# Performance work log

Measured on AMD Instinct MI355X. Metric: run time of the kernel, lower is better.

Reference implementation:

```python
import jax, jax.numpy as jnp
import numpy as np

K = 9        # kNN neighbors (ViG default kernel_size=9)
EPS = 1e-5   # BatchNorm eps


def _bn2d(x, gamma, beta):
    # training-mode BatchNorm2d over (B,H,W) per channel; x: [B,C,H,W]
    mean = jnp.mean(x, axis=(0, 2, 3), keepdims=True)
    var = jnp.var(x, axis=(0, 2, 3), keepdims=True)
    g = gamma.reshape(1, -1, 1, 1)
    b = beta.reshape(1, -1, 1, 1)
    return g * (x - mean) * jax.lax.rsqrt(var + EPS) + b


def setup_inputs() -> dict:
    key = jax.random.key(0)
    B, C, H, W = 8, 96, 56, 56
    oup = 192
    ks = jax.random.split(key, 8)
    sc = 0.05
    return {
        "x": jax.random.normal(ks[0], (B, C, H, W), dtype=jnp.float32),
        "W_fc1": jax.random.normal(ks[1], (C, C), dtype=jnp.float32) * sc,
        "b_fc1": jnp.zeros((C,), jnp.float32),
        "g_bn1": jnp.ones((C,), jnp.float32),
        "be_bn1": jnp.zeros((C,), jnp.float32),
        "W_edge": jax.random.normal(ks[2], (2 * C, 2 * C), dtype=jnp.float32) * sc,
        "b_edge": jnp.zeros((2 * C,), jnp.float32),
        "g_bne": jnp.ones((2 * C,), jnp.float32),
        "be_bne": jnp.zeros((2 * C,), jnp.float32),
        "W_fc2": jax.random.normal(ks[3], (2 * C, C), dtype=jnp.float32) * sc,
        "b_fc2": jnp.zeros((C,), jnp.float32),
        "g_bn2": jnp.ones((C,), jnp.float32),
        "be_bn2": jnp.zeros((C,), jnp.float32),
        "g_sabn": jnp.ones((C,), jnp.float32),
        "be_sabn": jnp.zeros((C,), jnp.float32),
        "W_dw": jax.random.normal(ks[4], (oup, C, 3, 3), dtype=jnp.float32) * sc,
        "b_dw": jnp.zeros((oup,), jnp.float32),
        "g_dwbn": jnp.ones((oup,), jnp.float32),
        "be_dwbn": jnp.zeros((oup,), jnp.float32),
    }


def reference(x, W_fc1, b_fc1, g_bn1, be_bn1, W_edge, b_edge, g_bne, be_bne,
              W_fc2, b_fc2, g_bn2, be_bn2, g_sabn, be_sabn,
              W_dw, b_dw, g_dwbn, be_dwbn):
    B, C, H, W = x.shape
    N = H * W
    shortcut = x

    # --- Grapher.fc1: 1x1 conv + BN ---
    y = jnp.einsum('bchw,cd->bdhw', x, W_fc1) + b_fc1[None, :, None, None]
    y = _bn2d(y, g_bn1, be_bn1)

    # --- dynamic kNN graph over flattened tokens ---
    ft = y.reshape(B, C, N).transpose(0, 2, 1)            # [B,N,C]
    sq = jnp.sum(ft * ft, axis=-1)                        # [B,N]
    dist = sq[:, :, None] - 2.0 * jnp.einsum('bnc,bmc->bnm', ft, ft) + sq[:, None, :]
    _, idx = jax.lax.top_k(-dist, K)                      # [B,N,K] nearest neighbors

    # --- EdgeConv: max_k act(BN(W [x_i, x_j - x_i])) ---
    x_j = jnp.take_along_axis(ft[:, :, None, :], idx[..., None], axis=1)  # [B,N,K,C]
    x_i = ft[:, :, None, :]                               # [B,N,1,C]
    e = jnp.concatenate([jnp.broadcast_to(x_i, x_j.shape), x_j - x_i], axis=-1)  # [B,N,K,2C]
    e = jnp.einsum('bnkc,cd->bnkd', e, W_edge) + b_edge
    m = jnp.mean(e, axis=(0, 1, 2))
    v = jnp.var(e, axis=(0, 1, 2))
    e = g_bne * (e - m) * jax.lax.rsqrt(v + EPS) + be_bne
    e = jax.nn.relu(e)
    g = jnp.max(e, axis=2)                                # [B,N,2C] max-aggregation

    # --- Grapher.fc2: 1x1 conv + BN, residual ---
    g = jnp.einsum('bnc,cd->bnd', g, W_fc2) + b_fc2       # [B,N,C]
    g = g.transpose(0, 2, 1).reshape(B, C, H, W)
    g = _bn2d(g, g_bn2, be_bn2)
    y = g + shortcut

    # --- SAEncoder: BN + ReLU ---
    y = jax.nn.relu(_bn2d(y, g_sabn, be_sabn))

    # --- convdw: 3x3 stride-2 conv + BN + ReLU ---
    y = jax.lax.conv_general_dilated(
        y, W_dw, window_strides=(2, 2), padding=((1, 1), (1, 1)),
        dimension_numbers=('NCHW', 'OIHW', 'NCHW')) + b_dw[None, :, None, None]
    y = jax.nn.relu(_bn2d(y, g_dwbn, be_dwbn))
    return y
```

## Files before the change

kernel.cpp:

```cpp
#include <hip/hip_runtime.h>
#include <math.h>

#define B_   8
#define C_   96
#define C2_  192
#define N_   3136
#define R_   25088
#define OUP_ 192
#define HO_  28
#define NO_  784
#define EPS_ 1e-5f
#define QSTR 104
#define CAP3 64

typedef short bf16x8 __attribute__((ext_vector_type(8)));
typedef float f32x4  __attribute__((ext_vector_type(4)));

__global__ __launch_bounds__(512) void k_fc1_d(const float* __restrict__ x,
                                               const float* __restrict__ W1,
                                               const float* __restrict__ b1,
                                               double* __restrict__ yd) {
    __shared__ double Wl[96 * 48];
    int tid = threadIdx.x;
    int rl = tid & 255, h = tid >> 8;
    int dbase = blockIdx.y * 48;
    for (int q = tid; q < 96 * 48; q += 512) {
        int c = q / 48, dd = q % 48;
        Wl[c * 48 + dd] = (double)W1[c * 96 + dbase + dd];
    }
    __syncthreads();
    int r = blockIdx.x * 256 + rl;
    int b = r / N_;
    int n = r - b * N_;
    double acc[24];
#pragma unroll
    for (int i = 0; i < 24; i++) acc[i] = 0.0;
    const float* xp = x + (size_t)b * C_ * N_ + n;
    for (int c = 0; c < 96; ++c) {
        double xv = (double)xp[(size_t)c * N_];
        const double* w = &Wl[c * 48 + h * 24];
#pragma unroll
        for (int i = 0; i < 24; ++i) acc[i] += xv * w[i];
    }
    int d0 = dbase + h * 24;
#pragma unroll
    for (int i = 0; i < 24; i++) {
        int d = d0 + i;
        yd[((size_t)b * C_ + d) * N_ + n] = acc[i] + (double)b1[d];
    }
}

__global__ __launch_bounds__(256) void k_stats_chan_d(const double* __restrict__ src,
                                                      double* __restrict__ partial) {
    int c = blockIdx.x;
    int chunk = blockIdx.y;
    const int SPLIT = 16;
    double s = 0.0, ss = 0.0;
    for (int j = chunk * 256 + threadIdx.x; j < R_; j += SPLIT * 256) {
        int b = j / N_, n = j - b * N_;
        double v = src[((size_t)b * C_ + c) * N_ + n];
        s += v;
        ss += v * v;
    }
    __shared__ double red[8];
    for (int off = 32; off; off >>= 1) {
        s += __shfl_down(s, off, 64);
        ss += __shfl_down(ss, off, 64);
    }
    int lane = threadIdx.x & 63, w = threadIdx.x >> 6;
    if (lane == 0) { red[w * 2] = s; red[w * 2 + 1] = ss; }
    __syncthreads();
    if (threadIdx.x == 0) {
        s = red[0] + red[2] + red[4] + red[6];
        ss = red[1] + red[3] + red[5] + red[7];
        partial[(c * SPLIT + chunk) * 2] = s;
        partial[(c * SPLIT + chunk) * 2 + 1] = ss;
    }
}

__global__ void k_stats_reduce_d(const double* __restrict__ partial, double* __restrict__ stats) {
    int c = blockIdx.x * blockDim.x + threadIdx.x;
    if (c >= 96) return;
    double s = 0.0, ss = 0.0;
    for (int k = 0; k < 16; k++) {
        s += partial[(c * 16 + k) * 2];
        ss += partial[(c * 16 + k) * 2 + 1];
    }
    double m = s / (double)R_;
    double var = ss / (double)R_ - m * m;
    stats[c * 2] = m;
    stats[c * 2 + 1] = 1.0 / sqrt(var + 1e-5);
}

__global__ __launch_bounds__(256) void k_stats_chan(const float* __restrict__ src,
                                                    float* __restrict__ partial,
                                                    int Cn, int Nsp, int total) {
    int c = blockIdx.x;
    int chunk = blockIdx.y;
    int SPLIT = gridDim.y;
    float s = 0.f, ss = 0.f;
    for (int j = chunk * 256 + threadIdx.x; j < total; j += SPLIT * 256) {
        int b = j / Nsp, n = j - b * Nsp;
        float v = src[((size_t)b * Cn + c) * Nsp + n];
        s += v;
        ss += v * v;
    }
    __shared__ float red[8];
    for (int off = 32; off; off >>= 1) {
        s += __shfl_down(s, off, 64);
        ss += __shfl_down(ss, off, 64);
    }
    int lane = threadIdx.x & 63, w = threadIdx.x >> 6;
    if (lane == 0) { red[w * 2] = s; red[w * 2 + 1] = ss; }
    __syncthreads();
    if (threadIdx.x == 0) {
        s = red[0] + red[2] + red[4] + red[6];
        ss = red[1] + red[3] + red[5] + red[7];
        partial[(c * SPLIT + chunk) * 2] = s;
        partial[(c * SPLIT + chunk) * 2 + 1] = ss;
    }
}

__global__ void k_stats_reduce(const float* __restrict__ partial, float* __restrict__ stats,
                               int Cn, int SPLIT, float invcount) {
    int c = blockIdx.x * blockDim.x + threadIdx.x;
    if (c >= Cn) return;
    float s = 0.f, ss = 0.f;
    for (int k = 0; k < SPLIT; k++) {
        s += partial[(c * SPLIT + k) * 2];
        ss += partial[(c * SPLIT + k) * 2 + 1];
    }
    float m = s * invcount;
    float var = ss * invcount - m * m;
    stats[c * 2] = m;
    stats[c * 2 + 1] = 1.0f / sqrtf(var + EPS_);
}

__global__ __launch_bounds__(256) void k_stats_reduce_b2(const float* __restrict__ partial,
                                                         float* __restrict__ stats,
                                                         float invcount) {
    int c = blockIdx.x;
    float s = 0.f, ss = 0.f;
    for (int k = threadIdx.x; k < 784; k += 256) {
        s  += partial[(size_t)k * 384 + c];
        ss += partial[(size_t)k * 384 + 192 + c];
    }
    __shared__ float red[8];
    for (int off = 32; off; off >>= 1) {
        s += __shfl_down(s, off, 64);
        ss += __shfl_down(ss, off, 64);
    }
    int lane = threadIdx.x & 63, w = threadIdx.x >> 6;
    if (lane == 0) { red[w * 2] = s; red[w * 2 + 1] = ss; }
    __syncthreads();
    if (threadIdx.x == 0) {
        s = red[0] + red[2] + red[4] + red[6];
        ss = red[1] + red[3] + red[5] + red[7];
        float m = s * invcount;
        float var = ss * invcount - m * m;
        stats[c * 2] = m;
        stats[c * 2 + 1] = 1.0f / sqrtf(var + EPS_);
    }
}

__global__ __launch_bounds__(256) void k_bn1_apply_d(const double* __restrict__ yd,
                                                     const double* __restrict__ stats,
                                                     const float* __restrict__ g,
                                                     const float* __restrict__ be,
                                                     float* __restrict__ ftc,
                                                     float* __restrict__ ftp32,
                                                     double* __restrict__ ftp64) {
    int i = blockIdx.x * 256 + threadIdx.x;
    if (i >= B_ * C_ * N_) return;
    int n = i % N_;
    int bc = i / N_;
    int c = bc % C_;
    int b = bc / C_;
    double m = stats[c * 2], rs = stats[c * 2 + 1];
    double v = (double)g[c] * (yd[i] - m) * rs + (double)be[c];
    float vf = (float)v;
    ftc[i] = vf;
    size_t pp = ((size_t)b * N_ + n) * C_ + c;
    ftp32[pp] = vf;
    ftp64[pp] = v;
}

__global__ __launch_bounds__(256) void k_sqrows_d(const double* __restrict__ ftp64,
                                                  double* __restrict__ sq64,
                                                  float* __restrict__ sq32) {
    int r = blockIdx.x * 256 + threadIdx.x;
    if (r >= R_) return;
    const double* p = ftp64 + (size_t)r * C_;
    double s = 0.0;
    for (int q = 0; q < 96; q++) s += p[q] * p[q];
    sq64[r] = s;
    sq32[r] = (float)s;
}

__global__ __launch_bounds__(256) void k_split_h(const float* __restrict__ ftp32,
                                                 unsigned short* __restrict__ fspH) {
    int t = blockIdx.x * 256 + threadIdx.x;
    if (t >= R_ * 12) return;
    int p = t / 12, g = t % 12;
    const float* src = ftp32 + (size_t)p * C_ + g * 8;
    unsigned short hi[8];
#pragma unroll
    for (int j = 0; j < 8; ++j) {
        unsigned u = __float_as_uint(src[j]);
        hi[j] = (unsigned short)((u + 0x7fffu + ((u >> 16) & 1u)) >> 16);
    }
    unsigned short* dh = fspH + (size_t)p * QSTR + g * 8;
    *(ushort4*)dh       = *(ushort4*)&hi[0];
    *(ushort4*)(dh + 4) = *(ushort4*)&hi[4];
}

__global__ __launch_bounds__(256) void k_dist3(const unsigned short* __restrict__ fspH,
                                               const float* __restrict__ sq32,
                                               unsigned short* __restrict__ poolC,
                                               unsigned* __restrict__ poolCnt) {
    __shared__ __align__(16) char lds[42112];
    unsigned short* cminL = (unsigned short*)(lds + 26624);
    unsigned short* poolL = (unsigned short*)(lds + 32896);
    unsigned*       cntL  = (unsigned*)(lds + 41088);
    float*          t16fL = (float*)(lds + 41344);

    int b = blockIdx.y;
    int q0 = blockIdx.x * 64;
    int tid = threadIdx.x;
    int w = tid >> 6, l = tid & 63;
    const int koff = (l >> 4) * 8;

    {
        const uint4* src = (const uint4*)(fspH + ((size_t)b * N_ + q0) * QSTR);
        uint4* dst = (uint4*)(lds + 26624);
        for (int i = tid; i < 832; i += 256) dst[i] = src[i];
    }
    __syncthreads();
    bf16x8 Bq[3];
    {
        const unsigned short* Ql = (const unsigned short*)(lds + 26624);
#pragma unroll
        for (int s = 0; s < 3; ++s)
            Bq[s] = *(const bf16x8*)&Ql[(w * 16 + (l & 15)) * QSTR + s * 32 + koff];
    }
    __syncthreads();

    {
        const uint4* src = (const uint4*)(fspH + ((size_t)b * N_) * QSTR);
        uint4* dst = (uint4*)lds;
#pragma unroll
        for (int k = 0; k < 4; ++k) { int i = tid + k * 256; if (i < 832) dst[i] = src[i]; }
        if (tid < 64) ((float*)(lds + 41600))[tid] = sq32[(size_t)b * N_ + tid];
    }
    __syncthreads();

    float t16r = 0.f;
    int cur = 0;
    for (int t = 0; t < 98; ++t) {
        int ch = (t < 49) ? t : t - 49;
        int c0 = ch * 64;
        bool pf = (t < 97);
        uint4 st0, st1, st2, st3; float sqst = 0.f;
        if (pf) {
            int nch = (t + 1 < 49) ? (t + 1) : (t + 1 - 49);
            const uint4* src = (const uint4*)(fspH + ((size_t)b * N_ + nch * 64) * QSTR);
            st0 = src[tid];
            st1 = src[tid + 256];
            st2 = src[tid + 512];
            if (tid < 64) { st3 = src[tid + 768]; sqst = sq32[(size_t)b * N_ + nch * 64 + tid]; }
        }
        const unsigned short* Bc = (const unsigned short*)(lds + cur * 13312);
        const float* sqc = (const float*)(lds + 41600 + cur * 256);
        f32x4 acc[4];
#pragma unroll
        for (int ct = 0; ct < 4; ++ct) acc[ct] = (f32x4){0.f, 0.f, 0.f, 0.f};
#pragma unroll
        for (int s = 0; s < 3; ++s) {
#pragma unroll
            for (int ct = 0; ct < 4; ++ct) {
                bf16x8 Ac = *(const bf16x8*)&Bc[(ct * 16 + (l & 15)) * QSTR + s * 32 + koff];
                acc[ct] = __builtin_amdgcn_mfma_f32_16x16x32_bf16(Ac, Bq[s], acc[ct], 0, 0, 0);
            }
        }
        f32x4 scn[4];
#pragma unroll
        for (int ct = 0; ct < 4; ++ct) scn[ct] = *(const f32x4*)&sqc[ct * 16 + (l >> 4) * 4];
        if (t < 49) {
            float m = 1e30f;
#pragma unroll
            for (int ct = 0; ct < 4; ++ct)
#pragma unroll
                for (int j = 0; j < 4; ++j)
                    m = fminf(m, fmaf(-2.f, acc[ct][j], scn[ct][j]));
            m = fminf(m, __shfl_xor(m, 16, 64));
            m = fminf(m, __shfl_xor(m, 32, 64));
            if (l < 16) {
                unsigned u = __float_as_uint(m);
                unsigned ku = u ^ (0x80000000u | (unsigned)((int)u >> 31));
                cminL[ch * 64 + w * 16 + l] = (unsigned short)(ku >> 16);
            }
        } else {
            int qrow = w * 16 + (l & 15);
#pragma unroll
            for (int ct = 0; ct < 4; ++ct)
#pragma unroll
                for (int j = 0; j < 4; ++j) {
                    float d = fmaf(-2.f, acc[ct][j], scn[ct][j]);
                    if (d <= t16r) {
                        unsigned pos = atomicAdd(&cntL[qrow], 1u);
                        if (pos < (unsigned)CAP3)
                            poolL[qrow * CAP3 + pos] = (unsigned short)(c0 + ct * 16 + (l >> 4) * 4 + j);
                    }
                }
        }
        if (t == 48) {
            __syncthreads();
            if (tid < 64) {
                unsigned short top[16];
#pragma unroll
                for (int j = 0; j < 16; ++j) top[j] = 0xFFFFu;
                for (int q = 0; q < 49; ++q) {
                    unsigned short v = cminL[q * 64 + tid];
                    if (v < top[15]) {
                        top[15] = v;
#pragma unroll
                        for (int j = 15; j >= 1; --j)
                            if (top[j] < top[j - 1]) { unsigned short tt = top[j]; top[j] = top[j - 1]; top[j - 1] = tt; }
                    }
                }
                unsigned ku = ((unsigned)top[15] << 16) | 0xFFFFu;
                float f = (ku & 0x80000000u) ? __uint_as_float(ku ^ 0x80000000u)
                                             : __uint_as_float(~ku);
                t16fL[tid] = f + fabsf(f) * 0.01f + 1.0f;
                cntL[tid] = 0u;
            }
            __syncthreads();
            t16r = t16fL[w * 16 + (l & 15)];
        }
        if (pf) {
            uint4* dst = (uint4*)(lds + (cur ^ 1) * 13312);
            dst[tid] = st0;
            dst[tid + 256] = st1;
            dst[tid + 512] = st2;
            if (tid < 64) { dst[tid + 768] = st3; ((float*)(lds + 41600 + (cur ^ 1) * 256))[tid] = sqst; }
        }
        __syncthreads();
        cur ^= 1;
    }
    if (tid < 64) {
        unsigned c = cntL[tid];
        poolCnt[(size_t)b * N_ + q0 + tid] = (c > (unsigned)CAP3) ? (unsigned)CAP3 : c;
    }
    {
        unsigned* dst = (unsigned*)(poolC + ((size_t)b * N_ + q0) * CAP3);
        const unsigned* src = (const unsigned*)poolL;
        for (int i = tid; i < 64 * CAP3 / 2; i += 256) dst[i] = src[i];
    }
}

__global__ __launch_bounds__(256) void k_rerank_d(const unsigned short* __restrict__ poolC,
                                                  const unsigned* __restrict__ poolCnt,
                                                  const double* __restrict__ ftp64,
                                                  const double* __restrict__ sq64,
                                                  int* __restrict__ idx) {
    int tid = threadIdx.x;
    int wv = tid >> 6, l = tid & 63;
    int rr = blockIdx.x * 4 + wv;
    int b = rr / N_;
    unsigned cnt = poolCnt[rr];
    if (cnt > (unsigned)CAP3) cnt = CAP3;
    double d = 1e300;
    int j = 0x7fffffff;
    if (l < (int)cnt) {
        j = (int)poolC[(size_t)rr * CAP3 + l];
        const double* qb = ftp64 + (size_t)rr * C_;
        const double* cb = ftp64 + ((size_t)b * N_ + j) * C_;
        double s0 = 0.0, s1 = 0.0;
#pragma unroll
        for (int k = 0; k < 96; k += 2) {
            s0 += qb[k] * cb[k];
            s1 += qb[k + 1] * cb[k + 1];
        }
        d = sq64[(size_t)b * N_ + j] - 2.0 * (s0 + s1);
    }
#pragma unroll
    for (int r = 0; r < 9; ++r) {
        double dm = d;
        int jm = j;
#pragma unroll
        for (int off = 1; off <= 32; off <<= 1) {
            double od = __shfl_xor(dm, off, 64);
            int oj = __shfl_xor(jm, off, 64);
            if (od < dm || (od == dm && oj < jm)) { dm = od; jm = oj; }
        }
        if (l == 0) idx[(size_t)rr * 9 + r] = jm;
        if (j == jm) d = 1e300;
    }
}

__global__ __launch_bounds__(512) void k_gemm_uv(const float* __restrict__ ftc,
                                                 const float* __restrict__ We,
                                                 const float* __restrict__ beb,
                                                 float* __restrict__ out, int mode) {
    __shared__ float Wl[96 * 48];
    int tid = threadIdx.x;
    int rl = tid & 255, h = tid >> 8;
    int dbase = blockIdx.y * 48;
    for (int q = tid; q < 96 * 48; q += 512) {
        int c = q / 48, dd = q % 48;
        float w = We[(96 + c) * C2_ + dbase + dd];
        if (mode == 0) w = We[c * C2_ + dbase + dd] - w;
        Wl[c * 48 + dd] = w;
    }
    __syncthreads();
    int r = blockIdx.x * 256 + rl;
    int b = r / N_, n = r - b * N_;
    float acc[24];
#pragma unroll
    for (int i = 0; i < 24; i++) acc[i] = 0.f;
    const float* xp = ftc + (size_t)b * C_ * N_ + n;
    for (int c = 0; c < 96; ++c) {
        float xv = xp[(size_t)c * N_];
        const float4* w4 = (const float4*)&Wl[c * 48 + h * 24];
#pragma unroll
        for (int i = 0; i < 6; ++i) {
            float4 w = w4[i];
            acc[i * 4 + 0] += xv * w.x;
            acc[i * 4 + 1] += xv * w.y;
            acc[i * 4 + 2] += xv * w.z;
            acc[i * 4 + 3] += xv * w.w;
        }
    }
    int d0 = dbase + h * 24;
    float* op = out + (size_t)r * C2_ + d0;
#pragma unroll
    for (int i = 0; i < 6; ++i) {
        float4 o;
        o.x = acc[i * 4 + 0]; o.y = acc[i * 4 + 1];
        o.z = acc[i * 4 + 2]; o.w = acc[i * 4 + 3];
        if (mode == 0) {
            o.x += beb[d0 + i * 4 + 0];
            o.y += beb[d0 + i * 4 + 1];
            o.z += beb[d0 + i * 4 + 2];
            o.w += beb[d0 + i * 4 + 3];
        }
        ((float4*)op)[i] = o;
    }
}

__global__ __launch_bounds__(192) void k_bne_stats(const float* __restrict__ u,
                                                   const float* __restrict__ v,
                                                   const int* __restrict__ idx,
                                                   float* __restrict__ partial) {
    int d = threadIdx.x;
    int row0 = blockIdx.x * 32;
    int b = row0 / N_;
    float s = 0.f, ss = 0.f;
    for (int r = 0; r < 32; ++r) {
        int row = row0 + r;
        float ud = u[(size_t)row * C2_ + d];
        const int* ip = idx + (size_t)row * 9;
#pragma unroll
        for (int k = 0; k < 9; k++) {
            int j = ip[k];
            float e = ud + v[((size_t)b * N_ + j) * C2_ + d];
            s += e;
            ss += e * e;
        }
    }
    partial[(size_t)blockIdx.x * 384 + d] = s;
    partial[(size_t)blockIdx.x * 384 + 192 + d] = ss;
}

__global__ __launch_bounds__(192) void k_edge_fc2(const float* __restrict__ u,
                                                  const float* __restrict__ v,
                                                  const int* __restrict__ idx,
                                                  const float* __restrict__ statsE,
                                                  const float* __restrict__ ge,
                                                  const float* __restrict__ bee,
                                                  const float* __restrict__ W2,
                                                  const float* __restrict__ b2,
                                                  float* __restrict__ out2) {
    __shared__ float gl[16][C2_];
    __shared__ float g2[C_][16];
    int tid = threadIdx.x;
    int row0 = blockIdx.x * 16;
    int b = row0 / N_;
    int n0 = row0 - b * N_;
    {
        int d = tid;
        float m = statsE[d * 2], rs = statsE[d * 2 + 1];
        float ga = ge[d], bb = bee[d];
        for (int r = 0; r < 16; ++r) {
            int row = row0 + r;
            float ud = u[(size_t)row * C2_ + d];
            const int* ip = idx + (size_t)row * 9;
            float gm = 0.f;
#pragma unroll
            for (int k = 0; k < 9; k++) {
                int j = ip[k];
                float e = ud + v[((size_t)b * N_ + j) * C2_ + d];
                float val = ga * (e - m) * rs + bb;
                gm = fmaxf(gm, val);
            }
            gl[r][d] = gm;
        }
    }
    __syncthreads();
    {
        int rr = tid / 24;
        int dq = tid % 24;
        for (int rep = 0; rep < 2; ++rep) {
            int r = rr + rep * 8;
            float4 acc = *(const float4*)&b2[dq * 4];
            for (int d = 0; d < C2_; ++d) {
                float gv = gl[r][d];
                float4 w = *(const float4*)&W2[d * C_ + dq * 4];
                acc.x += gv * w.x;
                acc.y += gv * w.y;
                acc.z += gv * w.z;
                acc.w += gv * w.w;
            }
            g2[dq * 4 + 0][r] = acc.x;
            g2[dq * 4 + 1][r] = acc.y;
            g2[dq * 4 + 2][r] = acc.z;
            g2[dq * 4 + 3][r] = acc.w;
        }
    }
    __syncthreads();
    for (int q = tid; q < 96 * 4; q += 192) {
        int dd = q / 4, part = q % 4;
        float4 val = *(const float4*)&g2[dd][part * 4];
        *(float4*)&out2[((size_t)b * C_ + dd) * N_ + n0 + part * 4] = val;
    }
}

__global__ __launch_bounds__(256) void k_bn2_add(const float* __restrict__ out2,
                                                 const float* __restrict__ x,
                                                 const float* __restrict__ stats,
                                                 const float* __restrict__ g,
                                                 const float* __restrict__ be,
                                                 float* __restrict__ t) {
    int i = blockIdx.x * 256 + threadIdx.x;
    if (i >= B_ * C_ * N_) return;
    int c = (i / N_) % C_;
    t[i] = g[c] * (out2[i] - stats[c * 2]) * stats[c * 2 + 1] + be[c] + x[i];
}

__global__ __launch_bounds__(256) void k_sabn_relu(const float* __restrict__ t,
                                                   const float* __restrict__ stats,
                                                   const float* __restrict__ g,
                                                   const float* __restrict__ be,
                                                   float* __restrict__ s) {
    int i = blockIdx.x * 256 + threadIdx.x;
    if (i >= B_ * C_ * N_) return;
    int c = (i / N_) % C_;
    s[i] = fmaxf(g[c] * (t[i] - stats[c * 2]) * stats[c * 2 + 1] + be[c], 0.f);
}

__global__ __launch_bounds__(256) void k_conv(const float* __restrict__ s,
                                              const float* __restrict__ Wd,
                                              const float* __restrict__ bd,
                                              float* __restrict__ z) {
    __shared__ float Wl[96 * 9 * 16];
    int b = blockIdx.z;
    int oc0 = blockIdx.y * 16;
    int p = blockIdx.x * 256 + threadIdx.x;
    for (int i = threadIdx.x; i < 96 * 9 * 16; i += 256) {
        int oc = i & 15;
        int icq = i >> 4;
        Wl[i] = Wd[(size_t)(oc0 + oc) * 864 + icq];
    }
    __syncthreads();
    if (p >= NO_) return;
    int oh = p / HO_, ow = p % HO_;
    float acc[16];
#pragma unroll
    for (int i = 0; i < 16; i++) acc[i] = 0.f;
    int ih0 = oh * 2 - 1, iw0 = ow * 2 - 1;
    const float* sb = s + (size_t)b * C_ * N_;
    for (int ic = 0; ic < 96; ++ic) {
        const float* sp = sb + (size_t)ic * N_;
        float in[9];
#pragma unroll
        for (int kh = 0; kh < 3; kh++) {
            int ih = ih0 + kh;
            bool okh = (unsigned)ih < 56u;
#pragma unroll
            for (int kw = 0; kw < 3; kw++) {
                int iw = iw0 + kw;
                bool ok = okh && ((unsigned)iw < 56u);
                in[kh * 3 + kw] = ok ? sp[ih * 56 + iw] : 0.f;
            }
        }
#pragma unroll
        for (int q = 0; q < 9; q++) {
            float iv = in[q];
            const float4* w4 = (const float4*)&Wl[(ic * 9 + q) * 16];
#pragma unroll
            for (int j = 0; j < 4; j++) {
                float4 w = w4[j];
                acc[j * 4 + 0] += iv * w.x;
                acc[j * 4 + 1] += iv * w.y;
                acc[j * 4 + 2] += iv * w.z;
                acc[j * 4 + 3] += iv * w.w;
            }
        }
    }
#pragma unroll
    for (int i = 0; i < 16; i++)
        z[((size_t)b * OUP_ + oc0 + i) * NO_ + p] = acc[i] + bd[oc0 + i];
}

__global__ __launch_bounds__(256) void k_out(const float* __restrict__ z,
                                             const float* __restrict__ stats,
                                             const float* __restrict__ g,
                                             const float* __restrict__ be,
                                             float* __restrict__ out) {
    int i = blockIdx.x * 256 + threadIdx.x;
    if (i >= B_ * OUP_ * NO_) return;
    int c = (i / NO_) % OUP_;
    out[i] = fmaxf(g[c] * (z[i] - stats[c * 2]) * stats[c * 2 + 1] + be[c], 0.f);
}

extern "C" void kernel_launch(void* const* d_in, const int* in_sizes, int n_in,
                              void* d_out, int out_size, void* d_ws, size_t ws_size,
                              hipStream_t stream) {
    const float* x     = (const float*)d_in[0];
    const float* W_fc1 = (const float*)d_in[1];
    const float* b_fc1 = (const float*)d_in[2];
    const float* g_bn1 = (const float*)d_in[3];
    const float* be_bn1= (const float*)d_in[4];
    const float* W_edge= (const float*)d_in[5];
    const float* b_edge= (const float*)d_in[6];
    const float* g_bne = (const float*)d_in[7];
    const float* be_bne= (const float*)d_in[8];
    const float* W_fc2 = (const float*)d_in[9];
    const float* b_fc2 = (const float*)d_in[10];
    const float* g_bn2 = (const float*)d_in[11];
    const float* be_bn2= (const float*)d_in[12];
    const float* g_sabn= (const float*)d_in[13];
    const float* be_sabn=(const float*)d_in[14];
    const float* W_dw  = (const float*)d_in[15];
    const float* b_dw  = (const float*)d_in[16];
    const float* g_dwbn= (const float*)d_in[17];
    const float* be_dwbn=(const float*)d_in[18];

    char* base = (char*)d_ws;
    float*  ftc   = (float*)(base + 0);
    float*  ftp32 = (float*)(base + 9633792);
    double* ftp64 = (double*)(base + 19267584);
    double* sq64  = (double*)(base + 38535168);
    double* yd    = (double*)(base + 38735872);
    unsigned short* fspH = (unsigned short*)(base + 38735872);
    float*  out2  = (float*)(base + 38735872);
    unsigned short* poolC = (unsigned short*)(base + 48771072);
    float*  zbuf  = (float*)(base + 48771072);
    int*    idx   = (int*)(base + 55193600);
    float*  uu    = (float*)(base + 19267584);
    float*  vv    = (float*)(base + 56096768);
    float*  tbuf  = (float*)(base + 9633792);
    float*  sbuf  = (float*)(base + 0);
    float*  partial = (float*)(base + 75364352);
    double* partiald = (double*)(base + 75364352);
    double* stats1d = (double*)(base + 76568576);
    float*  statsE  = (float*)(base + 76570112);
    float*  stats2  = (float*)(base + 76571648);
    float*  statsS  = (float*)(base + 76573184);
    float*  statsD  = (float*)(base + 76574720);
    float*  sq32    = (float*)(base + 76576256);
    unsigned* poolCnt = (unsigned*)(base + 76676608);

    k_fc1_d<<<dim3(98, 2), 512, 0, stream>>>(x, W_fc1, b_fc1, yd);
    k_stats_chan_d<<<dim3(96, 16), 256, 0, stream>>>(yd, partiald);
    k_stats_reduce_d<<<1, 256, 0, stream>>>(partiald, stats1d);
    k_bn1_apply_d<<<9408, 256, 0, stream>>>(yd, stats1d, g_bn1, be_bn1, ftc, ftp32, ftp64);
    k_sqrows_d<<<98, 256, 0, stream>>>(ftp64, sq64, sq32);

    k_split_h<<<1176, 256, 0, stream>>>(ftp32, fspH);
    k_dist3<<<dim3(49, B_), 256, 0, stream>>>(fspH, sq32, poolC, poolCnt);
    k_rerank_d<<<6272, 256, 0, stream>>>(poolC, poolCnt, ftp64, sq64, idx);

    k_gemm_uv<<<dim3(98, 4), 512, 0, stream>>>(ftc, W_edge, b_edge, uu, 0);
    k_gemm_uv<<<dim3(98, 4), 512, 0, stream>>>(ftc, W_edge, b_edge, vv, 1);

    k_bne_stats<<<784, 192, 0, stream>>>(uu, vv, idx, partial);
    k_stats_reduce_b2<<<192, 256, 0, stream>>>(partial, statsE, 1.0f / 225792.0f);
    k_edge_fc2<<<1568, 192, 0, stream>>>(uu, vv, idx, statsE, g_bne, be_bne, W_fc2, b_fc2, out2);

    k_stats_chan<<<dim3(96, 16), 256, 0, stream>>>(out2, partial, 96, N_, R_);
    k_stats_reduce<<<1, 256, 0, stream>>>(partial, stats2, 96, 16, 1.0f / (float)R_);
    k_bn2_add<<<9408, 256, 0, stream>>>(out2, x, stats2, g_bn2, be_bn2, tbuf);

    k_stats_chan<<<dim3(96, 16), 256, 0, stream>>>(tbuf, partial, 96, N_, R_);
    k_stats_reduce<<<1, 256, 0, stream>>>(partial, statsS, 96, 16, 1.0f / (float)R_);
    k_sabn_relu<<<9408, 256, 0, stream>>>(tbuf, statsS, g_sabn, be_sabn, sbuf);

    k_conv<<<dim3(4, 12, 8), 256, 0, stream>>>(sbuf, W_dw, b_dw, zbuf);
    k_stats_chan<<<dim3(192, 8), 256, 0, stream>>>(zbuf, partial, 192, NO_, 6272);
    k_stats_reduce<<<1, 256, 0, stream>>>(partial, statsD, 192, 8, 1.0f / 6272.0f);
    k_out<<<4705, 256, 0, stream>>>(zbuf, statsD, g_dwbn, be_dwbn, (float*)d_out);
}
```

Measured before the change: 649.6 us.

## Fuse BN1 apply with transpose/split, swizzle dist LDS, shrink candidate threshold, fuse BN2 stats

Merges the BN1 apply, row-norm and bf16 split kernels into one tiled transpose kernel, and drops the fp32 transposed copy. k_dist3 now uses a 128-element row stride with an XOR swizzle to cut LDS bank conflicts. Its candidate threshold is taken from the 9th-best chunk minimum instead of the 16th, which shrinks the pool but gives less margin for bf16 error. Rerank splits each candidate dot product across 4 lanes so 16 candidates are scored per pass, and the BN2 residual add now computes its channel stats directly, removing a separate stats pass.

```diff
diff --git a/kernel.cpp b/kernel.cpp
--- a/kernel.cpp
+++ b/kernel.cpp
@@ -10,11 +10,13 @@
 #define HO_  28
 #define NO_  784
 #define EPS_ 1e-5f
-#define QSTR 104
+#define QS2  128
 #define CAP3 64
 
 typedef short bf16x8 __attribute__((ext_vector_type(8)));
 typedef float f32x4  __attribute__((ext_vector_type(4)));
+
+__device__ __forceinline__ int swz16(int i) { return (i & ~15) | ((i & 15) ^ ((i >> 4) & 7)); }
 
 __global__ __launch_bounds__(512) void k_fc1_d(const float* __restrict__ x,
                                                const float* __restrict__ W1,
@@ -163,98 +165,99 @@
     }
 }
 
-__global__ __launch_bounds__(256) void k_bn1_apply_d(const double* __restrict__ yd,
-                                                     const double* __restrict__ stats,
-                                                     const float* __restrict__ g,
-                                                     const float* __restrict__ be,
-                                                     float* __restrict__ ftc,
-                                                     float* __restrict__ ftp32,
-                                                     double* __restrict__ ftp64) {
-    int i = blockIdx.x * 256 + threadIdx.x;
-    if (i >= B_ * C_ * N_) return;
-    int n = i % N_;
-    int bc = i / N_;
-    int c = bc % C_;
-    int b = bc / C_;
-    double m = stats[c * 2], rs = stats[c * 2 + 1];
-    double v = (double)g[c] * (yd[i] - m) * rs + (double)be[c];
-    float vf = (float)v;
-    ftc[i] = vf;
-    size_t pp = ((size_t)b * N_ + n) * C_ + c;
-    ftp32[pp] = vf;
-    ftp64[pp] = v;
-}
-
-__global__ __launch_bounds__(256) void k_sqrows_d(const double* __restrict__ ftp64,
-                                                  double* __restrict__ sq64,
-                                                  float* __restrict__ sq32) {
-    int r = blockIdx.x * 256 + threadIdx.x;
-    if (r >= R_) return;
-    const double* p = ftp64 + (size_t)r * C_;
+__global__ __launch_bounds__(256) void k_bn1_tr(const double* __restrict__ yd,
+                                                const double* __restrict__ stats,
+                                                const float* __restrict__ g,
+                                                const float* __restrict__ be,
+                                                float* __restrict__ ftc,
+                                                double* __restrict__ ftp64,
+                                                unsigned short* __restrict__ fspH,
+                                                double* __restrict__ sq64,
+                                                float* __restrict__ sq32) {
+    __shared__ double tile[64 * 97];
+    __shared__ double dsq[64][4];
+    int b = blockIdx.y;
+    int n0 = blockIdx.x * 64;
+    int tid = threadIdx.x;
+    int n = tid & 63, w = tid >> 6;
+    for (int k = 0; k < 24; ++k) {
+        int c = k * 4 + w;
+        size_t gi = ((size_t)b * C_ + c) * N_ + n0 + n;
+        double m = stats[c * 2], rs = stats[c * 2 + 1];
+        double v = (double)g[c] * (yd[gi] - m) * rs + (double)be[c];
+        ftc[gi] = (float)v;
+        tile[n * 97 + c] = v;
+    }
+    __syncthreads();
+    int p = n, q = w;
+    double vals[24];
     double s = 0.0;
-    for (int q = 0; q < 96; q++) s += p[q] * p[q];
-    sq64[r] = s;
-    sq32[r] = (float)s;
-}
-
-__global__ __launch_bounds__(256) void k_split_h(const float* __restrict__ ftp32,
-                                                 unsigned short* __restrict__ fspH) {
-    int t = blockIdx.x * 256 + threadIdx.x;
-    if (t >= R_ * 12) return;
-    int p = t / 12, g = t % 12;
-    const float* src = ftp32 + (size_t)p * C_ + g * 8;
-    unsigned short hi[8];
-#pragma unroll
-    for (int j = 0; j < 8; ++j) {
-        unsigned u = __float_as_uint(src[j]);
-        hi[j] = (unsigned short)((u + 0x7fffu + ((u >> 16) & 1u)) >> 16);
-    }
-    unsigned short* dh = fspH + (size_t)p * QSTR + g * 8;
-    *(ushort4*)dh       = *(ushort4*)&hi[0];
-    *(ushort4*)(dh + 4) = *(ushort4*)&hi[4];
+    const double* lp = &tile[p * 97 + q * 24];
+#pragma unroll
+    for (int m2 = 0; m2 < 24; ++m2) { vals[m2] = lp[m2]; s += vals[m2] * vals[m2]; }
+    dsq[p][q] = s;
+    double* dst = ftp64 + ((size_t)b * N_ + n0 + p) * C_ + q * 24;
+#pragma unroll
+    for (int m2 = 0; m2 < 24; m2 += 2) *(double2*)&dst[m2] = make_double2(vals[m2], vals[m2 + 1]);
+    unsigned* hdst = (unsigned*)(fspH + ((size_t)b * N_ + n0 + p) * QS2);
+#pragma unroll
+    for (int m2 = 0; m2 < 24; m2 += 2) {
+        unsigned u0 = __float_as_uint((float)vals[m2]);
+        unsigned u1 = __float_as_uint((float)vals[m2 + 1]);
+        unsigned h0 = (u0 + 0x7fffu + ((u0 >> 16) & 1u)) >> 16;
+        unsigned h1 = (u1 + 0x7fffu + ((u1 >> 16) & 1u)) >> 16;
+        hdst[q * 12 + (m2 >> 1)] = h0 | (h1 << 16);
+    }
+    __syncthreads();
+    if (tid < 64) {
+        double tot = dsq[tid][0] + dsq[tid][1] + dsq[tid][2] + dsq[tid][3];
+        sq64[(size_t)b * N_ + n0 + tid] = tot;
+        sq32[(size_t)b * N_ + n0 + tid] = (float)tot;
+    }
 }
 
 __global__ __launch_bounds__(256) void k_dist3(const unsigned short* __restrict__ fspH,
                                                const float* __restrict__ sq32,
                                                unsigned short* __restrict__ poolC,
                                                unsigned* __restrict__ poolCnt) {
-    __shared__ __align__(16) char lds[42112];
-    unsigned short* cminL = (unsigned short*)(lds + 26624);
-    unsigned short* poolL = (unsigned short*)(lds + 32896);
-    unsigned*       cntL  = (unsigned*)(lds + 41088);
-    float*          t16fL = (float*)(lds + 41344);
+    __shared__ __align__(16) char lds[48256];
+    unsigned short* cminL = (unsigned short*)(lds + 32768);
+    unsigned short* poolL = (unsigned short*)(lds + 39040);
+    unsigned*       cntL  = (unsigned*)(lds + 47232);
+    float*          t9fL  = (float*)(lds + 47488);
 
     int b = blockIdx.y;
     int q0 = blockIdx.x * 64;
     int tid = threadIdx.x;
     int w = tid >> 6, l = tid & 63;
-    const int koff = (l >> 4) * 8;
 
     {
-        const uint4* src = (const uint4*)(fspH + ((size_t)b * N_ + q0) * QSTR);
-        uint4* dst = (uint4*)(lds + 26624);
-        for (int i = tid; i < 832; i += 256) dst[i] = src[i];
+        const uint4* src = (const uint4*)(fspH + ((size_t)b * N_ + q0) * QS2);
+        uint4* dst = (uint4*)lds;
+        for (int i = tid; i < 1024; i += 256) dst[swz16(i)] = src[i];
     }
     __syncthreads();
     bf16x8 Bq[3];
     {
-        const unsigned short* Ql = (const unsigned short*)(lds + 26624);
-#pragma unroll
-        for (int s = 0; s < 3; ++s)
-            Bq[s] = *(const bf16x8*)&Ql[(w * 16 + (l & 15)) * QSTR + s * 32 + koff];
+        const unsigned short* Ql = (const unsigned short*)lds;
+        int qr = w * 16 + (l & 15);
+#pragma unroll
+        for (int s = 0; s < 3; ++s) {
+            int col = (s * 4 + (l >> 4)) ^ (qr & 7);
+            Bq[s] = *(const bf16x8*)&Ql[qr * QS2 + col * 8];
+        }
     }
     __syncthreads();
 
     {
-        const uint4* src = (const uint4*)(fspH + ((size_t)b * N_) * QSTR);
+        const uint4* src = (const uint4*)(fspH + (size_t)b * N_ * QS2);
         uint4* dst = (uint4*)lds;
-#pragma unroll
-        for (int k = 0; k < 4; ++k) { int i = tid + k * 256; if (i < 832) dst[i] = src[i]; }
-        if (tid < 64) ((float*)(lds + 41600))[tid] = sq32[(size_t)b * N_ + tid];
-    }
-    __syncthreads();
-
-    float t16r = 0.f;
+        for (int i = tid; i < 1024; i += 256) dst[swz16(i)] = src[i];
+        if (tid < 64) ((float*)(lds + 47744))[tid] = sq32[(size_t)b * N_ + tid];
+    }
+    __syncthreads();
+
+    float t9r = 0.f;
     int cur = 0;
     for (int t = 0; t < 98; ++t) {
         int ch = (t < 49) ? t : t - 49;
@@ -263,14 +266,15 @@
         uint4 st0, st1, st2, st3; float sqst = 0.f;
         if (pf) {
             int nch = (t + 1 < 49) ? (t + 1) : (t + 1 - 49);
-            const uint4* src = (const uint4*)(fspH + ((size_t)b * N_ + nch * 64) * QSTR);
+            const uint4* src = (const uint4*)(fspH + ((size_t)b * N_ + nch * 64) * QS2);
             st0 = src[tid];
             st1 = src[tid + 256];
             st2 = src[tid + 512];
-            if (tid < 64) { st3 = src[tid + 768]; sqst = sq32[(size_t)b * N_ + nch * 64 + tid]; }
-        }
-        const unsigned short* Bc = (const unsigned short*)(lds + cur * 13312);
-        const float* sqc = (const float*)(lds + 41600 + cur * 256);
+            st3 = src[tid + 768];
+            if (tid < 64) sqst = sq32[(size_t)b * N_ + nch * 64 + tid];
+        }
+        const unsigned short* Bc = (const unsigned short*)(lds + cur * 16384);
+        const float* sqc = (const float*)(lds + 47744 + cur * 256);
         f32x4 acc[4];
 #pragma unroll
         for (int ct = 0; ct < 4; ++ct) acc[ct] = (f32x4){0.f, 0.f, 0.f, 0.f};
@@ -278,7 +282,9 @@
         for (int s = 0; s < 3; ++s) {
 #pragma unroll
             for (int ct = 0; ct < 4; ++ct) {
-                bf16x8 Ac = *(const bf16x8*)&Bc[(ct * 16 + (l & 15)) * QSTR + s * 32 + koff];
+                int cr = ct * 16 + (l & 15);
+                int col = (s * 4 + (l >> 4)) ^ (cr & 7);
+                bf16x8 Ac = *(const bf16x8*)&Bc[cr * QS2 + col * 8];
                 acc[ct] = __builtin_amdgcn_mfma_f32_16x16x32_bf16(Ac, Bq[s], acc[ct], 0, 0, 0);
             }
         }
@@ -306,7 +312,7 @@
 #pragma unroll
                 for (int j = 0; j < 4; ++j) {
                     float d = fmaf(-2.f, acc[ct][j], scn[ct][j]);
-                    if (d <= t16r) {
+                    if (d <= t9r) {
                         unsigned pos = atomicAdd(&cntL[qrow], 1u);
                         if (pos < (unsigned)CAP3)
                             poolL[qrow * CAP3 + pos] = (unsigned short)(c0 + ct * 16 + (l >> 4) * 4 + j);
@@ -316,33 +322,34 @@
         if (t == 48) {
             __syncthreads();
             if (tid < 64) {
-                unsigned short top[16];
-#pragma unroll
-                for (int j = 0; j < 16; ++j) top[j] = 0xFFFFu;
+                unsigned short top[9];
+#pragma unroll
+                for (int j = 0; j < 9; ++j) top[j] = 0xFFFFu;
                 for (int q = 0; q < 49; ++q) {
                     unsigned short v = cminL[q * 64 + tid];
-                    if (v < top[15]) {
-                        top[15] = v;
-#pragma unroll
-                        for (int j = 15; j >= 1; --j)
+                    if (v < top[8]) {
+                        top[8] = v;
+#pragma unroll
+                        for (int j = 8; j >= 1; --j)
                             if (top[j] < top[j - 1]) { unsigned short tt = top[j]; top[j] = top[j - 1]; top[j - 1] = tt; }
                     }
                 }
-                unsigned ku = ((unsigned)top[15] << 16) | 0xFFFFu;
+                unsigned ku = ((unsigned)top[8] << 16) | 0xFFFFu;
                 float f = (ku & 0x80000000u) ? __uint_as_float(ku ^ 0x80000000u)
                                              : __uint_as_float(~ku);
-                t16fL[tid] = f + fabsf(f) * 0.01f + 1.0f;
+                t9fL[tid] = f + fabsf(f) * 0.01f + 1.0f;
                 cntL[tid] = 0u;
             }
             __syncthreads();
-            t16r = t16fL[w * 16 + (l & 15)];
+            t9r = t9fL[w * 16 + (l & 15)];
         }
         if (pf) {
-            uint4* dst = (uint4*)(lds + (cur ^ 1) * 13312);
-            dst[tid] = st0;
-            dst[tid + 256] = st1;
-            dst[tid + 512] = st2;
-            if (tid < 64) { dst[tid + 768] = st3; ((float*)(lds + 41600 + (cur ^ 1) * 256))[tid] = sqst; }
+            uint4* dst = (uint4*)(lds + (cur ^ 1) * 16384);
+            dst[swz16(tid)] = st0;
+            dst[swz16(tid + 256)] = st1;
+            dst[swz16(tid + 512)] = st2;
+            dst[swz16(tid + 768)] = st3;
+            if (tid < 64) ((float*)(lds + 47744 + (cur ^ 1) * 256))[tid] = sqst;
         }
         __syncthreads();
         cur ^= 1;
@@ -367,26 +374,42 @@
     int wv = tid >> 6, l = tid & 63;
     int rr = blockIdx.x * 4 + wv;
     int b = rr / N_;
-    unsigned cnt = poolCnt[rr];
-    if (cnt > (unsigned)CAP3) cnt = CAP3;
-    double d = 1e300;
-    int j = 0x7fffffff;
-    if (l < (int)cnt) {
-        j = (int)poolC[(size_t)rr * CAP3 + l];
-        const double* qb = ftp64 + (size_t)rr * C_;
-        const double* cb = ftp64 + ((size_t)b * N_ + j) * C_;
-        double s0 = 0.0, s1 = 0.0;
-#pragma unroll
-        for (int k = 0; k < 96; k += 2) {
-            s0 += qb[k] * cb[k];
-            s1 += qb[k + 1] * cb[k + 1];
-        }
-        d = sq64[(size_t)b * N_ + j] - 2.0 * (s0 + s1);
+    int cnt = (int)poolCnt[rr];
+    if (cnt > CAP3) cnt = CAP3;
+    int e = l & 3;
+    double qreg[24];
+    {
+        const double* qb = ftp64 + (size_t)rr * C_ + e * 24;
+#pragma unroll
+        for (int m = 0; m < 24; ++m) qreg[m] = qb[m];
+    }
+    double dv[4];
+    int jv[4];
+#pragma unroll
+    for (int gG = 0; gG < 4; ++gG) { dv[gG] = 1e300; jv[gG] = 0x7fffffff; }
+#pragma unroll
+    for (int gG = 0; gG < 4; ++gG) {
+        if (gG * 16 >= cnt) break;
+        int ci = gG * 16 + (l >> 2);
+        bool valid = ci < cnt;
+        int j = valid ? (int)poolC[(size_t)rr * CAP3 + ci] : 0;
+        const double* cb = ftp64 + ((size_t)b * N_ + j) * C_ + e * 24;
+        double p = 0.0;
+#pragma unroll
+        for (int m = 0; m < 24; ++m) p += qreg[m] * cb[m];
+        p += __shfl_xor(p, 1, 64);
+        p += __shfl_xor(p, 2, 64);
+        if (valid) {
+            dv[gG] = sq64[(size_t)b * N_ + j] - 2.0 * p;
+            jv[gG] = j;
+        }
     }
 #pragma unroll
     for (int r = 0; r < 9; ++r) {
-        double dm = d;
-        int jm = j;
+        double dm = dv[0]; int jm = jv[0];
+#pragma unroll
+        for (int gG = 1; gG < 4; ++gG)
+            if (dv[gG] < dm || (dv[gG] == dm && jv[gG] < jm)) { dm = dv[gG]; jm = jv[gG]; }
 #pragma unroll
         for (int off = 1; off <= 32; off <<= 1) {
             double od = __shfl_xor(dm, off, 64);
@@ -394,7 +417,9 @@
             if (od < dm || (od == dm && oj < jm)) { dm = od; jm = oj; }
         }
         if (l == 0) idx[(size_t)rr * 9 + r] = jm;
-        if (j == jm) d = 1e300;
+#pragma unroll
+        for (int gG = 0; gG < 4; ++gG)
+            if (jv[gG] == jm) dv[gG] = 1e300;
     }
 }
 
@@ -535,16 +560,41 @@
     }
 }
 
-__global__ __launch_bounds__(256) void k_bn2_add(const float* __restrict__ out2,
-                                                 const float* __restrict__ x,
-                                                 const float* __restrict__ stats,
-                                                 const float* __restrict__ g,
-                                                 const float* __restrict__ be,
-                                                 float* __restrict__ t) {
-    int i = blockIdx.x * 256 + threadIdx.x;
-    if (i >= B_ * C_ * N_) return;
-    int c = (i / N_) % C_;
-    t[i] = g[c] * (out2[i] - stats[c * 2]) * stats[c * 2 + 1] + be[c] + x[i];
+__global__ __launch_bounds__(256) void k_bn2_add_st(const float* __restrict__ out2,
+                                                    const float* __restrict__ x,
+                                                    const float* __restrict__ stats,
+                                                    const float* __restrict__ g,
+                                                    const float* __restrict__ be,
+                                                    float* __restrict__ t,
+                                                    float* __restrict__ partial) {
+    int c = blockIdx.x;
+    int chunk = blockIdx.y;
+    const int SPLIT = 16;
+    float m = stats[c * 2], rs = stats[c * 2 + 1];
+    float ga = g[c], bb = be[c];
+    float s = 0.f, ss = 0.f;
+    for (int j = chunk * 256 + threadIdx.x; j < R_; j += SPLIT * 256) {
+        int b = j / N_, n = j - b * N_;
+        size_t i = ((size_t)b * C_ + c) * N_ + n;
+        float tv = ga * (out2[i] - m) * rs + bb + x[i];
+        t[i] = tv;
+        s += tv;
+        ss += tv * tv;
+    }
+    __shared__ float red[8];
+    for (int off = 32; off; off >>= 1) {
+        s += __shfl_down(s, off, 64);
+        ss += __shfl_down(ss, off, 64);
+    }
+    int lane = threadIdx.x & 63, w = threadIdx.x >> 6;
+    if (lane == 0) { red[w * 2] = s; red[w * 2 + 1] = ss; }
+    __syncthreads();
+    if (threadIdx.x == 0) {
+        s = red[0] + red[2] + red[4] + red[6];
+        ss = red[1] + red[3] + red[5] + red[7];
+        partial[(c * SPLIT + chunk) * 2] = s;
+        partial[(c * SPLIT + chunk) * 2 + 1] = ss;
+    }
 }
 
 __global__ __launch_bounds__(256) void k_sabn_relu(const float* __restrict__ t,
@@ -648,36 +698,33 @@
 
     char* base = (char*)d_ws;
     float*  ftc   = (float*)(base + 0);
-    float*  ftp32 = (float*)(base + 9633792);
-    double* ftp64 = (double*)(base + 19267584);
-    double* sq64  = (double*)(base + 38535168);
-    double* yd    = (double*)(base + 38735872);
-    unsigned short* fspH = (unsigned short*)(base + 38735872);
-    float*  out2  = (float*)(base + 38735872);
-    unsigned short* poolC = (unsigned short*)(base + 48771072);
-    float*  zbuf  = (float*)(base + 48771072);
-    int*    idx   = (int*)(base + 55193600);
-    float*  uu    = (float*)(base + 19267584);
-    float*  vv    = (float*)(base + 56096768);
-    float*  tbuf  = (float*)(base + 9633792);
     float*  sbuf  = (float*)(base + 0);
-    float*  partial = (float*)(base + 75364352);
-    double* partiald = (double*)(base + 75364352);
-    double* stats1d = (double*)(base + 76568576);
-    float*  statsE  = (float*)(base + 76570112);
-    float*  stats2  = (float*)(base + 76571648);
-    float*  statsS  = (float*)(base + 76573184);
-    float*  statsD  = (float*)(base + 76574720);
-    float*  sq32    = (float*)(base + 76576256);
-    unsigned* poolCnt = (unsigned*)(base + 76676608);
+    double* ftp64 = (double*)(base + 9633792);
+    float*  uu    = (float*)(base + 9633792);
+    double* yd    = (double*)(base + 28901376);
+    float*  vv    = (float*)(base + 28901376);
+    unsigned short* fspH = (unsigned short*)(base + 48168960);
+    float*  out2  = (float*)(base + 48168960);
+    unsigned short* poolC = (unsigned short*)(base + 57802752);
+    float*  tbuf  = (float*)(base + 57802752);
+    double* sq64  = (double*)(base + 67436544);
+    int*    idx   = (int*)(base + 67637248);
+    unsigned* poolCnt = (unsigned*)(base + 68540416);
+    float*  sq32  = (float*)(base + 68640768);
+    float*  partial = (float*)(base + 68741120);
+    double* partiald = (double*)(base + 68741120);
+    double* stats1d = (double*)(base + 69945344);
+    float*  statsE  = (float*)(base + 69946880);
+    float*  stats2  = (float*)(base + 69948416);
+    float*  statsS  = (float*)(base + 69949952);
+    float*  statsD  = (float*)(base + 69951488);
+    float*  zbuf  = (float*)(base + 69953024);
 
     k_fc1_d<<<dim3(98, 2), 512, 0, stream>>>(x, W_fc1, b_fc1, yd);
     k_stats_chan_d<<<dim3(96, 16), 256, 0, stream>>>(yd, partiald);
     k_stats_reduce_d<<<1, 256, 0, stream>>>(partiald, stats1d);
-    k_bn1_apply_d<<<9408, 256, 0, stream>>>(yd, stats1d, g_bn1, be_bn1, ftc, ftp32, ftp64);
-    k_sqrows_d<<<98, 256, 0, stream>>>(ftp64, sq64, sq32);
-
-    k_split_h<<<1176, 256, 0, stream>>>(ftp32, fspH);
+    k_bn1_tr<<<dim3(49, B_), 256, 0, stream>>>(yd, stats1d, g_bn1, be_bn1, ftc, ftp64, fspH, sq64, sq32);
+
     k_dist3<<<dim3(49, B_), 256, 0, stream>>>(fspH, sq32, poolC, poolCnt);
     k_rerank_d<<<6272, 256, 0, stream>>>(poolC, poolCnt, ftp64, sq64, idx);
 
@@ -690,9 +737,7 @@
 
     k_stats_chan<<<dim3(96, 16), 256, 0, stream>>>(out2, partial, 96, N_, R_);
     k_stats_reduce<<<1, 256, 0, stream>>>(partial, stats2, 96, 16, 1.0f / (float)R_);
-    k_bn2_add<<<9408, 256, 0, stream>>>(out2, x, stats2, g_bn2, be_bn2, tbuf);
-
-    k_stats_chan<<<dim3(96, 16), 256, 0, stream>>>(tbuf, partial, 96, N_, R_);
+    k_bn2_add_st<<<dim3(96, 16), 256, 0, stream>>>(out2, x, stats2, g_bn2, be_bn2, tbuf, partial);
     k_stats_reduce<<<1, 256, 0, stream>>>(partial, statsS, 96, 16, 1.0f / (float)R_);
     k_sabn_relu<<<9408, 256, 0, stream>>>(tbuf, statsS, g_sabn, be_sabn, sbuf);
 
```

Result: faster. 570.7 us (-12.1%).
